# Performance work log

Measured on AMD Instinct MI355X. Metric: run time of the kernel, lower is better.

Reference implementation:

```python
import jax, jax.numpy as jnp
import numpy as np

EPS = 1e-5
LORA_DIM = 64
LORA_SCALE = LORA_DIM ** (-0.5)
GRAD_SCALE = 0.5  # infeat_grad_scale (bp_to_unet=True path)


def _ln(x, g=None, b=None):
    mu = jnp.mean(x, axis=-1, keepdims=True)
    var = jnp.mean((x - mu) ** 2, axis=-1, keepdims=True)
    y = (x - mu) * jax.lax.rsqrt(var + EPS)
    if g is not None:
        y = y * g + b
    return y


def _grad_scale(t, s=GRAD_SCALE):
    # identity in forward, scales gradient by s in backward
    return t * s + jax.lax.stop_gradient(t) * (1.0 - s)


def setup_inputs() -> dict:
    key = jax.random.key(0)
    ks = jax.random.split(key, 8)
    B, C, H, W = 32, 1280, 32, 32
    TD, LD = 768, LORA_DIM
    inp = {}
    inp["layer_infeat"] = jax.random.normal(ks[0], (B, C, H, W), jnp.float32)
    inp["layer_inquery"] = jax.random.normal(ks[1], (B, H * W, C), jnp.float32)
    inp["token_q_emb"] = jax.random.normal(ks[2], (TD,), jnp.float32)
    # learned params
    inp["to_q_w"] = jax.random.normal(ks[3], (C, TD), jnp.float32) * (TD ** -0.5)
    inp["ln_x_g"] = jnp.ones((C,), jnp.float32)
    inp["ln_x_b"] = jnp.zeros((C,), jnp.float32)
    inp["ln_k_g"] = jnp.ones((C,), jnp.float32)
    inp["ln_k_b"] = jnp.zeros((C,), jnp.float32)
    inp["ln_q_g"] = jnp.ones((TD,), jnp.float32)
    inp["ln_q_b"] = jnp.zeros((TD,), jnp.float32)
    inp["lora_q_w"] = jax.random.normal(ks[4], (LD, C), jnp.float32) * (C ** -0.5)
    inp["lora_k_w"] = jax.random.normal(ks[5], (LD, C), jnp.float32) * (C ** -0.5)
    inp["mask"] = jax.random.randint(ks[6], (B, 1, H, W), 0, 2).astype(jnp.float32)
    return inp


def reference(layer_infeat, layer_inquery, token_q_emb, to_q_w,
              ln_x_g, ln_x_b, ln_k_g, ln_k_b, ln_q_g, ln_q_b,
              lora_q_w, lora_k_w, mask):
    B, C, H, W = layer_infeat.shape
    # flatten(2).permute(0,2,1): [B,C,H,W] -> [B, HW, C]
    x = _grad_scale(layer_infeat).reshape(B, C, H * W).transpose(0, 2, 1)
    k_in = _grad_scale(layer_inquery)
    # q = to_q(ln_q(token_q_emb[None])) -> [1, C], broadcast to [B, 1, C]
    q = _ln(token_q_emb[None, :], ln_q_g, ln_q_b) @ to_q_w.T
    q = jnp.broadcast_to(q[None], (B, 1, C))
    k = _ln(k_in, ln_k_g, ln_k_b)   # [B, HW, C]
    v = _ln(x, ln_x_g, ln_x_b)      # [B, HW, C]
    # LoRA score path (use_lora=True since lora_dim>0)
    lora_q = _ln(q) @ lora_q_w.T    # [B, 1, LD]
    lora_k = _ln(k) @ lora_k_w.T    # [B, HW, LD]
    sim = jnp.einsum('bid,bjd->bij', lora_q, lora_k) * LORA_SCALE  # [B,1,HW]
    # mask: nearest interpolation to (H,W) is identity (same size); flatten
    m = mask.reshape(B, 1, H * W) > 0
    sim = jnp.where(m, sim, -jnp.finfo(sim.dtype).max)
    attn = jax.nn.softmax(sim, axis=-1)
    fg = jnp.einsum('bij,bjd->bid', attn, v)            # [B, 1, C]
    bg = jnp.mean(v, axis=1, keepdims=True) - fg        # [B, 1, C]
    out = jnp.concatenate([fg, bg], axis=-1)            # [B, 1, 2C]
    return out[:, 0, :]                                  # [B, 2C]
```

## Files before the change

### kernel.cpp

```cpp
#include <hip/hip_runtime.h>
#include <math.h>

#define B_   32
#define CD   1280
#define HW_  1024
#define TD_  768
#define LD_  64
#define EPSF 1e-5f
#define LORA_SCALE_F 0.125f

__device__ __forceinline__ float wredSum(float a) {
#pragma unroll
  for (int o = 32; o; o >>= 1) a += __shfl_xor(a, o, 64);
  return a;
}
__device__ __forceinline__ void wred2(float& a, float& b) {
#pragma unroll
  for (int o = 32; o; o >>= 1) { a += __shfl_xor(a, o, 64); b += __shfl_xor(b, o, 64); }
}
__device__ __forceinline__ float blockSum(float v, float* red) {
  int t = threadIdx.x;
  red[t] = v; __syncthreads();
#pragma unroll
  for (int s = 128; s > 0; s >>= 1) { if (t < s) red[t] += red[t + s]; __syncthreads(); }
  float r = red[0]; __syncthreads();
  return r;
}
__device__ __forceinline__ float blockMax(float v, float* red) {
  int t = threadIdx.x;
  red[t] = v; __syncthreads();
#pragma unroll
  for (int s = 128; s > 0; s >>= 1) { if (t < s) red[t] = fmaxf(red[t], red[t + s]); __syncthreads(); }
  float r = red[0]; __syncthreads();
  return r;
}
__device__ __forceinline__ void blockSum2(float& a, float& b, float2* red) {
  int t = threadIdx.x;
  red[t] = make_float2(a, b); __syncthreads();
#pragma unroll
  for (int s = 128; s > 0; s >>= 1) {
    if (t < s) { red[t].x += red[t + s].x; red[t].y += red[t + s].y; }
    __syncthreads();
  }
  a = red[0].x; b = red[0].y; __syncthreads();
}

__global__ __launch_bounds__(256) void kA12(const float* __restrict__ tq,
                                            const float* __restrict__ lng,
                                            const float* __restrict__ lnb,
                                            const float* __restrict__ to_q_w,
                                            float* __restrict__ q_out) {
  __shared__ float lnq[TD_];
  __shared__ float2 red[256];
  int t = threadIdx.x;
  float s = 0.f, ss = 0.f, vals[3];
#pragma unroll
  for (int k = 0; k < 3; k++) { float v = tq[t + 256 * k]; vals[k] = v; s += v; ss += v * v; }
  blockSum2(s, ss, red);
  float mu = s * (1.f / TD_);
  float r = rsqrtf(ss * (1.f / TD_) - mu * mu + EPSF);
#pragma unroll
  for (int k = 0; k < 3; k++) { int i = t + 256 * k; lnq[i] = (vals[k] - mu) * r * lng[i] + lnb[i]; }
  __syncthreads();
  int c = blockIdx.x * 4 + (t >> 6);
  int lane = t & 63;
  const float4* w4 = (const float4*)(to_q_w + (size_t)c * TD_);
  const float4* l4 = (const float4*)lnq;
  float dot = 0.f;
#pragma unroll
  for (int i = 0; i < 3; i++) {
    int f = i * 64 + lane;
    float4 w = w4[f], l = l4[f];
    dot += w.x * l.x + w.y * l.y + w.z * l.z + w.w * l.w;
  }
  dot = wredSum(dot);
  if (lane == 0) q_out[c] = dot;
}

__global__ __launch_bounds__(256) void kA34(const float* __restrict__ q_in,
                                            const float* __restrict__ lora_q_w,
                                            float* __restrict__ lq_out) {
  __shared__ float qs[CD];
  __shared__ float2 red[256];
  int t = threadIdx.x;
  float s = 0.f, ss = 0.f, vals[5];
#pragma unroll
  for (int k = 0; k < 5; k++) { float v = q_in[t + 256 * k]; vals[k] = v; s += v; ss += v * v; }
  blockSum2(s, ss, red);
  float mu = s * (1.f / CD);
  float r = rsqrtf(ss * (1.f / CD) - mu * mu + EPSF);
#pragma unroll
  for (int k = 0; k < 5; k++) { int i = t + 256 * k; qs[i] = (vals[k] - mu) * r; }
  __syncthreads();
  int d = blockIdx.x * 4 + (t >> 6);
  int lane = t & 63;
  const float4* w4 = (const float4*)(lora_q_w + (size_t)d * CD);
  const float4* q4 = (const float4*)qs;
  float dot = 0.f;
#pragma unroll
  for (int i = 0; i < 5; i++) {
    int f = i * 64 + lane;
    float4 w = w4[f], qq = q4[f];
    dot += w.x * qq.x + w.y * qq.y + w.z * qq.z + w.w * qq.w;
  }
  dot = wredSum(dot);
  if (lane == 0) lq_out[d] = dot;
}

__global__ __launch_bounds__(256) void kA56(const float* __restrict__ lq,
                                            const float* __restrict__ lora_k_w,
                                            float* __restrict__ w_eff) {
  __shared__ float l[LD_];
  int t = threadIdx.x;
  if (t < LD_) l[t] = lq[t];
  __syncthreads();
  int c = blockIdx.x * 256 + t;
  float acc = 0.f;
#pragma unroll 8
  for (int d = 0; d < LD_; d++) acc += l[d] * lora_k_w[(size_t)d * CD + c];
  w_eff[c] = acc;
}

__global__ __launch_bounds__(256) void kB(const float* __restrict__ kin,
                                          const float* __restrict__ g,
                                          const float* __restrict__ bb,
                                          const float* __restrict__ w_eff,
                                          float* __restrict__ sim) {
  __shared__ float4 gs[CD / 4], bs[CD / 4], ws[CD / 4];
  __shared__ float red[256];
  int t = threadIdx.x;
  float wsum = 0.f;
  for (int k = t; k < CD / 4; k += 256) {
    float4 w = ((const float4*)w_eff)[k];
    ws[k] = w;
    gs[k] = ((const float4*)g)[k];
    bs[k] = ((const float4*)bb)[k];
    wsum += w.x + w.y + w.z + w.w;
  }
  float W0 = blockSum(wsum, red);
  int wid = t >> 6, lane = t & 63;
  int gw = blockIdx.x * 4 + wid;
  for (int row = gw; row < B_ * HW_; row += 8192) {
    const float4* x4 = (const float4*)(kin + (size_t)row * CD);
    float4 xv[5];
    float s = 0.f, ss = 0.f;
#pragma unroll
    for (int i = 0; i < 5; i++) {
      float4 v = x4[i * 64 + lane];
      xv[i] = v;
      s += v.x + v.y + v.z + v.w;
      ss += v.x * v.x + v.y * v.y + v.z * v.z + v.w * v.w;
    }
    wred2(s, ss);
    float mu1 = s * (1.f / CD);
    float r1 = rsqrtf(ss * (1.f / CD) - mu1 * mu1 + EPSF);
    float s2 = 0.f, ss2 = 0.f;
#pragma unroll
    for (int i = 0; i < 5; i++) {
      int f = i * 64 + lane;
      float4 G = gs[f], Bv = bs[f], v = xv[i], kk;
      kk.x = (v.x - mu1) * r1 * G.x + Bv.x;
      kk.y = (v.y - mu1) * r1 * G.y + Bv.y;
      kk.z = (v.z - mu1) * r1 * G.z + Bv.z;
      kk.w = (v.w - mu1) * r1 * G.w + Bv.w;
      xv[i] = kk;
      s2 += kk.x + kk.y + kk.z + kk.w;
      ss2 += kk.x * kk.x + kk.y * kk.y + kk.z * kk.z + kk.w * kk.w;
    }
    wred2(s2, ss2);
    float mu2 = s2 * (1.f / CD);
    float r2 = rsqrtf(ss2 * (1.f / CD) - mu2 * mu2 + EPSF);
    float dot = 0.f;
#pragma unroll
    for (int i = 0; i < 5; i++) {
      float4 w = ws[i * 64 + lane], kk = xv[i];
      dot += w.x * kk.x + w.y * kk.y + w.z * kk.z + w.w * kk.w;
    }
    dot = wredSum(dot);
    if (lane == 0) sim[row] = LORA_SCALE_F * r2 * (dot - mu2 * W0);
  }
}

__global__ __launch_bounds__(256) void kD1(const float* __restrict__ infeat,
                                           float* __restrict__ mu_out,
                                           float* __restrict__ r_out) {
  int tile = blockIdx.x & 15, b = blockIdx.x >> 4;
  int t = threadIdx.x;
  int jg = t & 15;
  int slice = t >> 4;
  int j0 = tile * 64 + jg * 4;
  const float* base = infeat + (size_t)b * CD * HW_ + j0;
  float4 s = make_float4(0, 0, 0, 0), q = make_float4(0, 0, 0, 0);
  int c0 = slice * 80;
#pragma unroll 4
  for (int c = c0; c < c0 + 80; c++) {
    float4 v = *(const float4*)(base + (size_t)c * HW_);
    s.x += v.x; s.y += v.y; s.z += v.z; s.w += v.w;
    q.x += v.x * v.x; q.y += v.y * v.y; q.z += v.z * v.z; q.w += v.w * v.w;
  }
  __shared__ float4 sArr[16][16], qArr[16][16];
  sArr[slice][jg] = s; qArr[slice][jg] = q;
  __syncthreads();
#pragma unroll
  for (int st = 8; st > 0; st >>= 1) {
    if (slice < st) {
      float4 a = sArr[slice][jg], b2 = sArr[slice + st][jg];
      a.x += b2.x; a.y += b2.y; a.z += b2.z; a.w += b2.w;
      sArr[slice][jg] = a;
      a = qArr[slice][jg]; b2 = qArr[slice + st][jg];
      a.x += b2.x; a.y += b2.y; a.z += b2.z; a.w += b2.w;
      qArr[slice][jg] = a;
    }
    __syncthreads();
  }
  if (slice == 0) {
    float4 S = sArr[0][jg], Q = qArr[0][jg], mu, r;
    mu.x = S.x * (1.f / CD); mu.y = S.y * (1.f / CD);
    mu.z = S.z * (1.f / CD); mu.w = S.w * (1.f / CD);
    r.x = rsqrtf(Q.x * (1.f / CD) - mu.x * mu.x + EPSF);
    r.y = rsqrtf(Q.y * (1.f / CD) - mu.y * mu.y + EPSF);
    r.z = rsqrtf(Q.z * (1.f / CD) - mu.z * mu.z + EPSF);
    r.w = rsqrtf(Q.w * (1.f / CD) - mu.w * mu.w + EPSF);
    int j = b * HW_ + j0;
    *(float4*)(mu_out + j) = mu;
    *(float4*)(r_out + j) = r;
  }
}

__global__ __launch_bounds__(256) void kC(const float* __restrict__ sim,
                                          const float* __restrict__ mask,
                                          const float* __restrict__ mu,
                                          const float* __restrict__ r,
                                          float* __restrict__ w1,
                                          float* __restrict__ w2,
                                          float* __restrict__ S1,
                                          float* __restrict__ S3) {
  __shared__ float red[256];
  __shared__ float2 red2[256];
  int b = blockIdx.x, t = threadIdx.x;
  float4 sv = ((const float4*)(sim + b * HW_))[t];
  float4 mv = ((const float4*)(mask + b * HW_))[t];
  float4 muv = ((const float4*)(mu + b * HW_))[t];
  float4 rv = ((const float4*)(r + b * HW_))[t];
  const float NEG = -3.4028235e38f;
  float se0 = mv.x > 0.f ? sv.x : NEG;
  float se1 = mv.y > 0.f ? sv.y : NEG;
  float se2 = mv.z > 0.f ? sv.z : NEG;
  float se3 = mv.w > 0.f ? sv.w : NEG;
  float m = fmaxf(fmaxf(se0, se1), fmaxf(se2, se3));
  float M = blockMax(m, red);
  float e0 = expf(se0 - M), e1 = expf(se1 - M), e2 = expf(se2 - M), e3 = expf(se3 - M);
  float Z = blockSum(e0 + e1 + e2 + e3, red);
  float inv = 1.f / Z;
  float a0 = e0 * inv, a1 = e1 * inv, a2 = e2 * inv, a3 = e3 * inv;
  float4 w1v = make_float4(a0 * rv.x, a1 * rv.y, a2 * rv.z, a3 * rv.w);
  float4 w2v = make_float4(rv.x * (1.f / HW_), rv.y * (1.f / HW_),
                           rv.z * (1.f / HW_), rv.w * (1.f / HW_));
  float s1 = w1v.x * muv.x + w1v.y * muv.y + w1v.z * muv.z + w1v.w * muv.w;
  float s3 = w2v.x * muv.x + w2v.y * muv.y + w2v.z * muv.z + w2v.w * muv.w;
  blockSum2(s1, s3, red2);
  ((float4*)(w1 + b * HW_))[t] = w1v;
  ((float4*)(w2 + b * HW_))[t] = w2v;
  if (t == 0) { S1[b] = s1; S3[b] = s3; }
}

__global__ __launch_bounds__(256) void kD2(const float* __restrict__ infeat,
                                           const float* __restrict__ w1,
                                           const float* __restrict__ w2,
                                           const float* __restrict__ S1,
                                           const float* __restrict__ S3,
                                           const float* __restrict__ g,
                                           const float* __restrict__ bb,
                                           float* __restrict__ out) {
  __shared__ float4 w1s[HW_ / 4], w2s[HW_ / 4];
  int t = threadIdx.x;
  int b = blockIdx.x / 40, tile = blockIdx.x % 40;
  w1s[t] = ((const float4*)(w1 + b * HW_))[t];
  w2s[t] = ((const float4*)(w2 + b * HW_))[t];
  __syncthreads();
  int wid = t >> 6, lane = t & 63;
  float s1 = S1[b], s3 = S3[b];
#pragma unroll
  for (int k = 0; k < 8; k++) {
    int c = tile * 32 + wid * 8 + k;
    const float4* x4 = (const float4*)(infeat + (size_t)b * CD * HW_ + (size_t)c * HW_);
    float d1 = 0.f, d2 = 0.f;
#pragma unroll
    for (int i = 0; i < 4; i++) {
      int f = i * 64 + lane;
      float4 x = x4[f], a = w1s[f], w = w2s[f];
      d1 += x.x * a.x + x.y * a.y + x.z * a.z + x.w * a.w;
      d2 += x.x * w.x + x.y * w.y + x.z * w.z + x.w * w.w;
    }
    wred2(d1, d2);
    if (lane == 0) {
      float gc = g[c], bc = bb[c];
      float fg = gc * (d1 - s1) + bc;
      float vm = gc * (d2 - s3) + bc;
      out[(size_t)b * (2 * CD) + c] = fg;
      out[(size_t)b * (2 * CD) + CD + c] = vm - fg;
    }
  }
}

extern "C" void kernel_launch(void* const* d_in, const int* in_sizes, int n_in,
                              void* d_out, int out_size, void* d_ws, size_t ws_size,
                              hipStream_t stream) {
  const float* infeat  = (const float*)d_in[0];
  const float* inquery = (const float*)d_in[1];
  const float* tq      = (const float*)d_in[2];
  const float* to_q_w  = (const float*)d_in[3];
  const float* ln_x_g  = (const float*)d_in[4];
  const float* ln_x_b  = (const float*)d_in[5];
  const float* ln_k_g  = (const float*)d_in[6];
  const float* ln_k_b  = (const float*)d_in[7];
  const float* ln_q_g  = (const float*)d_in[8];
  const float* ln_q_b  = (const float*)d_in[9];
  const float* lora_q_w = (const float*)d_in[10];
  const float* lora_k_w = (const float*)d_in[11];
  const float* mask    = (const float*)d_in[12];
  float* out = (float*)d_out;

  float* ws = (float*)d_ws;
  float* q_ws    = ws;
  float* lq_ws   = ws + 1280;
  float* weff_ws = ws + 1344;
  float* sim_ws  = ws + 2624;
  float* mu_ws   = ws + 35392;
  float* r_ws    = ws + 68160;
  float* w1_ws   = ws + 100928;
  float* w2_ws   = ws + 133696;
  float* S1_ws   = ws + 166464;
  float* S3_ws   = ws + 166496;

  kA12<<<320, 256, 0, stream>>>(tq, ln_q_g, ln_q_b, to_q_w, q_ws);
  kA34<<<16, 256, 0, stream>>>(q_ws, lora_q_w, lq_ws);
  kA56<<<5, 256, 0, stream>>>(lq_ws, lora_k_w, weff_ws);
  kB<<<2048, 256, 0, stream>>>(inquery, ln_k_g, ln_k_b, weff_ws, sim_ws);
  kD1<<<512, 256, 0, stream>>>(infeat, mu_ws, r_ws);
  kC<<<32, 256, 0, stream>>>(sim_ws, mask, mu_ws, r_ws, w1_ws, w2_ws, S1_ws, S3_ws);
  kD2<<<1280, 256, 0, stream>>>(infeat, w1_ws, w2_ws, S1_ws, S3_ws, ln_x_g, ln_x_b, out);
}
```

Measured before the change: 405.7 us.

## Fuse small kernels: merge LoRA prep, co-schedule stats passes, fold softmax into final reduction

Merges the two LoRA projection kernels into one, in which each block recomputes the low-rank query vector. The key-path sim kernel and the infeat statistics kernel now run as one launch, split by block index, so the two independent memory-bound passes can overlap. The softmax/weight kernel is folded into the final reduction, with each of the 1280 blocks recomputing its batch's softmax weights in shared memory instead of reading them from a workspace. This cuts the launch count from seven to four and removes intermediate round trips, at the cost of redundant softmax and LoRA-q work per block.

```diff
diff --git a/kernel.cpp b/kernel.cpp
--- a/kernel.cpp
+++ b/kernel.cpp
@@ -18,19 +18,17 @@
 #pragma unroll
   for (int o = 32; o; o >>= 1) { a += __shfl_xor(a, o, 64); b += __shfl_xor(b, o, 64); }
 }
+__device__ __forceinline__ void wred3(float& a, float& b, float& c) {
+#pragma unroll
+  for (int o = 32; o; o >>= 1) {
+    a += __shfl_xor(a, o, 64); b += __shfl_xor(b, o, 64); c += __shfl_xor(c, o, 64);
+  }
+}
 __device__ __forceinline__ float blockSum(float v, float* red) {
   int t = threadIdx.x;
   red[t] = v; __syncthreads();
 #pragma unroll
   for (int s = 128; s > 0; s >>= 1) { if (t < s) red[t] += red[t + s]; __syncthreads(); }
-  float r = red[0]; __syncthreads();
-  return r;
-}
-__device__ __forceinline__ float blockMax(float v, float* red) {
-  int t = threadIdx.x;
-  red[t] = v; __syncthreads();
-#pragma unroll
-  for (int s = 128; s > 0; s >>= 1) { if (t < s) red[t] = fmaxf(red[t], red[t + s]); __syncthreads(); }
   float r = red[0]; __syncthreads();
   return r;
 }
@@ -77,167 +75,176 @@
   if (lane == 0) q_out[c] = dot;
 }
 
-__global__ __launch_bounds__(256) void kA34(const float* __restrict__ q_in,
-                                            const float* __restrict__ lora_q_w,
-                                            float* __restrict__ lq_out) {
-  __shared__ float qs[CD];
-  __shared__ float2 red[256];
-  int t = threadIdx.x;
+__global__ __launch_bounds__(256) void kA3456(const float* __restrict__ q_in,
+                                              const float* __restrict__ lora_q_w,
+                                              const float* __restrict__ lora_k_w,
+                                              float* __restrict__ w_eff) {
+  __shared__ float qn[CD];
+  __shared__ float lq[LD_];
+  __shared__ float redS[8];
+  int t = threadIdx.x;
+  int wid = t >> 6, lane = t & 63;
   float s = 0.f, ss = 0.f, vals[5];
 #pragma unroll
   for (int k = 0; k < 5; k++) { float v = q_in[t + 256 * k]; vals[k] = v; s += v; ss += v * v; }
-  blockSum2(s, ss, red);
+  wred2(s, ss);
+  if (lane == 0) { redS[wid * 2] = s; redS[wid * 2 + 1] = ss; }
+  __syncthreads();
+  s = redS[0] + redS[2] + redS[4] + redS[6];
+  ss = redS[1] + redS[3] + redS[5] + redS[7];
   float mu = s * (1.f / CD);
   float r = rsqrtf(ss * (1.f / CD) - mu * mu + EPSF);
 #pragma unroll
-  for (int k = 0; k < 5; k++) { int i = t + 256 * k; qs[i] = (vals[k] - mu) * r; }
-  __syncthreads();
-  int d = blockIdx.x * 4 + (t >> 6);
-  int lane = t & 63;
-  const float4* w4 = (const float4*)(lora_q_w + (size_t)d * CD);
-  const float4* q4 = (const float4*)qs;
-  float dot = 0.f;
-#pragma unroll
-  for (int i = 0; i < 5; i++) {
-    int f = i * 64 + lane;
-    float4 w = w4[f], qq = q4[f];
-    dot += w.x * qq.x + w.y * qq.y + w.z * qq.z + w.w * qq.w;
-  }
-  dot = wredSum(dot);
-  if (lane == 0) lq_out[d] = dot;
-}
-
-__global__ __launch_bounds__(256) void kA56(const float* __restrict__ lq,
-                                            const float* __restrict__ lora_k_w,
-                                            float* __restrict__ w_eff) {
-  __shared__ float l[LD_];
-  int t = threadIdx.x;
-  if (t < LD_) l[t] = lq[t];
+  for (int k = 0; k < 5; k++) { int i = t + 256 * k; qn[i] = (vals[k] - mu) * r; }
+  __syncthreads();
+  {
+    int g = t >> 2, sub = t & 3;
+    const float4* w4 = (const float4*)(lora_q_w + (size_t)g * CD);
+    const float4* q4 = (const float4*)qn;
+    float dot = 0.f;
+#pragma unroll 8
+    for (int i = 0; i < 80; i++) {
+      int f = i * 4 + sub;
+      float4 w = w4[f], qq = q4[f];
+      dot += w.x * qq.x + w.y * qq.y + w.z * qq.z + w.w * qq.w;
+    }
+    dot += __shfl_xor(dot, 1, 64);
+    dot += __shfl_xor(dot, 2, 64);
+    if (sub == 0) lq[g] = dot;
+  }
   __syncthreads();
   int c = blockIdx.x * 256 + t;
   float acc = 0.f;
 #pragma unroll 8
-  for (int d = 0; d < LD_; d++) acc += l[d] * lora_k_w[(size_t)d * CD + c];
+  for (int d = 0; d < LD_; d++) acc += lq[d] * lora_k_w[(size_t)d * CD + c];
   w_eff[c] = acc;
 }
 
-__global__ __launch_bounds__(256) void kB(const float* __restrict__ kin,
-                                          const float* __restrict__ g,
-                                          const float* __restrict__ bb,
-                                          const float* __restrict__ w_eff,
-                                          float* __restrict__ sim) {
-  __shared__ float4 gs[CD / 4], bs[CD / 4], ws[CD / 4];
-  __shared__ float red[256];
-  int t = threadIdx.x;
-  float wsum = 0.f;
-  for (int k = t; k < CD / 4; k += 256) {
-    float4 w = ((const float4*)w_eff)[k];
-    ws[k] = w;
-    gs[k] = ((const float4*)g)[k];
-    bs[k] = ((const float4*)bb)[k];
-    wsum += w.x + w.y + w.z + w.w;
-  }
-  float W0 = blockSum(wsum, red);
+__global__ __launch_bounds__(256) void kBD1(const float* __restrict__ kin,
+                                            const float* __restrict__ g,
+                                            const float* __restrict__ bb,
+                                            const float* __restrict__ w_eff,
+                                            float* __restrict__ sim,
+                                            const float* __restrict__ infeat,
+                                            float* __restrict__ mu_out,
+                                            float* __restrict__ r_out) {
+  __shared__ float4 smem[1024];
+  int t = threadIdx.x;
+  if (blockIdx.x < 2048) {
+    float4* gs = smem;
+    float4* bs = smem + 320;
+    float4* ws = smem + 640;
+    float* red = (float*)(smem + 960);
+    float wsum = 0.f;
+    for (int k = t; k < CD / 4; k += 256) {
+      float4 w = ((const float4*)w_eff)[k];
+      ws[k] = w;
+      gs[k] = ((const float4*)g)[k];
+      bs[k] = ((const float4*)bb)[k];
+      wsum += w.x + w.y + w.z + w.w;
+    }
+    float W0 = blockSum(wsum, red);
+    int wid = t >> 6, lane = t & 63;
+    int gw = blockIdx.x * 4 + wid;
+    for (int row = gw; row < B_ * HW_; row += 8192) {
+      const float4* x4 = (const float4*)(kin + (size_t)row * CD);
+      float4 xv[5];
+      float s = 0.f, ss = 0.f;
+#pragma unroll
+      for (int i = 0; i < 5; i++) {
+        float4 v = x4[i * 64 + lane];
+        xv[i] = v;
+        s += v.x + v.y + v.z + v.w;
+        ss += v.x * v.x + v.y * v.y + v.z * v.z + v.w * v.w;
+      }
+      wred2(s, ss);
+      float mu1 = s * (1.f / CD);
+      float r1 = rsqrtf(ss * (1.f / CD) - mu1 * mu1 + EPSF);
+      float s2 = 0.f, ss2 = 0.f;
+#pragma unroll
+      for (int i = 0; i < 5; i++) {
+        int f = i * 64 + lane;
+        float4 G = gs[f], Bv = bs[f], v = xv[i], kk;
+        kk.x = (v.x - mu1) * r1 * G.x + Bv.x;
+        kk.y = (v.y - mu1) * r1 * G.y + Bv.y;
+        kk.z = (v.z - mu1) * r1 * G.z + Bv.z;
+        kk.w = (v.w - mu1) * r1 * G.w + Bv.w;
+        xv[i] = kk;
+        s2 += kk.x + kk.y + kk.z + kk.w;
+        ss2 += kk.x * kk.x + kk.y * kk.y + kk.z * kk.z + kk.w * kk.w;
+      }
+      wred2(s2, ss2);
+      float mu2 = s2 * (1.f / CD);
+      float r2 = rsqrtf(ss2 * (1.f / CD) - mu2 * mu2 + EPSF);
+      float dot = 0.f;
+#pragma unroll
+      for (int i = 0; i < 5; i++) {
+        float4 w = ws[i * 64 + lane], kk = xv[i];
+        dot += w.x * kk.x + w.y * kk.y + w.z * kk.z + w.w * kk.w;
+      }
+      dot = wredSum(dot);
+      if (lane == 0) sim[row] = LORA_SCALE_F * r2 * (dot - mu2 * W0);
+    }
+  } else {
+    int blk = blockIdx.x - 2048;
+    int tile = blk & 15, b = blk >> 4;
+    int jg = t & 15;
+    int slice = t >> 4;
+    int j0 = tile * 64 + jg * 4;
+    const float* base = infeat + (size_t)b * CD * HW_ + j0;
+    float4 s = make_float4(0, 0, 0, 0), q = make_float4(0, 0, 0, 0);
+    int c0 = slice * 80;
+#pragma unroll 4
+    for (int c = c0; c < c0 + 80; c++) {
+      float4 v = *(const float4*)(base + (size_t)c * HW_);
+      s.x += v.x; s.y += v.y; s.z += v.z; s.w += v.w;
+      q.x += v.x * v.x; q.y += v.y * v.y; q.z += v.z * v.z; q.w += v.w * v.w;
+    }
+    float4* sArr = smem;
+    float4* qArr = smem + 256;
+    sArr[slice * 16 + jg] = s; qArr[slice * 16 + jg] = q;
+    __syncthreads();
+#pragma unroll
+    for (int st = 8; st > 0; st >>= 1) {
+      if (slice < st) {
+        float4 a = sArr[slice * 16 + jg], b2 = sArr[(slice + st) * 16 + jg];
+        a.x += b2.x; a.y += b2.y; a.z += b2.z; a.w += b2.w;
+        sArr[slice * 16 + jg] = a;
+        a = qArr[slice * 16 + jg]; b2 = qArr[(slice + st) * 16 + jg];
+        a.x += b2.x; a.y += b2.y; a.z += b2.z; a.w += b2.w;
+        qArr[slice * 16 + jg] = a;
+      }
+      __syncthreads();
+    }
+    if (slice == 0) {
+      float4 S = sArr[jg], Q = qArr[jg], mu, r;
+      mu.x = S.x * (1.f / CD); mu.y = S.y * (1.f / CD);
+      mu.z = S.z * (1.f / CD); mu.w = S.w * (1.f / CD);
+      r.x = rsqrtf(Q.x * (1.f / CD) - mu.x * mu.x + EPSF);
+      r.y = rsqrtf(Q.y * (1.f / CD) - mu.y * mu.y + EPSF);
+      r.z = rsqrtf(Q.z * (1.f / CD) - mu.z * mu.z + EPSF);
+      r.w = rsqrtf(Q.w * (1.f / CD) - mu.w * mu.w + EPSF);
+      int j = b * HW_ + j0;
+      *(float4*)(mu_out + j) = mu;
+      *(float4*)(r_out + j) = r;
+    }
+  }
+}
+
+__global__ __launch_bounds__(256) void kD2f(const float* __restrict__ infeat,
+                                            const float* __restrict__ sim,
+                                            const float* __restrict__ mask,
+                                            const float* __restrict__ mu,
+                                            const float* __restrict__ r,
+                                            const float* __restrict__ g,
+                                            const float* __restrict__ bb,
+                                            float* __restrict__ out) {
+  __shared__ float4 w1s[HW_ / 4], w2s[HW_ / 4];
+  __shared__ float red[16];
+  int t = threadIdx.x;
+  int b = blockIdx.x / 40, tile = blockIdx.x % 40;
   int wid = t >> 6, lane = t & 63;
-  int gw = blockIdx.x * 4 + wid;
-  for (int row = gw; row < B_ * HW_; row += 8192) {
-    const float4* x4 = (const float4*)(kin + (size_t)row * CD);
-    float4 xv[5];
-    float s = 0.f, ss = 0.f;
-#pragma unroll
-    for (int i = 0; i < 5; i++) {
-      float4 v = x4[i * 64 + lane];
-      xv[i] = v;
-      s += v.x + v.y + v.z + v.w;
-      ss += v.x * v.x + v.y * v.y + v.z * v.z + v.w * v.w;
-    }
-    wred2(s, ss);
-    float mu1 = s * (1.f / CD);
-    float r1 = rsqrtf(ss * (1.f / CD) - mu1 * mu1 + EPSF);
-    float s2 = 0.f, ss2 = 0.f;
-#pragma unroll
-    for (int i = 0; i < 5; i++) {
-      int f = i * 64 + lane;
-      float4 G = gs[f], Bv = bs[f], v = xv[i], kk;
-      kk.x = (v.x - mu1) * r1 * G.x + Bv.x;
-      kk.y = (v.y - mu1) * r1 * G.y + Bv.y;
-      kk.z = (v.z - mu1) * r1 * G.z + Bv.z;
-      kk.w = (v.w - mu1) * r1 * G.w + Bv.w;
-      xv[i] = kk;
-      s2 += kk.x + kk.y + kk.z + kk.w;
-      ss2 += kk.x * kk.x + kk.y * kk.y + kk.z * kk.z + kk.w * kk.w;
-    }
-    wred2(s2, ss2);
-    float mu2 = s2 * (1.f / CD);
-    float r2 = rsqrtf(ss2 * (1.f / CD) - mu2 * mu2 + EPSF);
-    float dot = 0.f;
-#pragma unroll
-    for (int i = 0; i < 5; i++) {
-      float4 w = ws[i * 64 + lane], kk = xv[i];
-      dot += w.x * kk.x + w.y * kk.y + w.z * kk.z + w.w * kk.w;
-    }
-    dot = wredSum(dot);
-    if (lane == 0) sim[row] = LORA_SCALE_F * r2 * (dot - mu2 * W0);
-  }
-}
-
-__global__ __launch_bounds__(256) void kD1(const float* __restrict__ infeat,
-                                           float* __restrict__ mu_out,
-                                           float* __restrict__ r_out) {
-  int tile = blockIdx.x & 15, b = blockIdx.x >> 4;
-  int t = threadIdx.x;
-  int jg = t & 15;
-  int slice = t >> 4;
-  int j0 = tile * 64 + jg * 4;
-  const float* base = infeat + (size_t)b * CD * HW_ + j0;
-  float4 s = make_float4(0, 0, 0, 0), q = make_float4(0, 0, 0, 0);
-  int c0 = slice * 80;
-#pragma unroll 4
-  for (int c = c0; c < c0 + 80; c++) {
-    float4 v = *(const float4*)(base + (size_t)c * HW_);
-    s.x += v.x; s.y += v.y; s.z += v.z; s.w += v.w;
-    q.x += v.x * v.x; q.y += v.y * v.y; q.z += v.z * v.z; q.w += v.w * v.w;
-  }
-  __shared__ float4 sArr[16][16], qArr[16][16];
-  sArr[slice][jg] = s; qArr[slice][jg] = q;
-  __syncthreads();
-#pragma unroll
-  for (int st = 8; st > 0; st >>= 1) {
-    if (slice < st) {
-      float4 a = sArr[slice][jg], b2 = sArr[slice + st][jg];
-      a.x += b2.x; a.y += b2.y; a.z += b2.z; a.w += b2.w;
-      sArr[slice][jg] = a;
-      a = qArr[slice][jg]; b2 = qArr[slice + st][jg];
-      a.x += b2.x; a.y += b2.y; a.z += b2.z; a.w += b2.w;
-      qArr[slice][jg] = a;
-    }
-    __syncthreads();
-  }
-  if (slice == 0) {
-    float4 S = sArr[0][jg], Q = qArr[0][jg], mu, r;
-    mu.x = S.x * (1.f / CD); mu.y = S.y * (1.f / CD);
-    mu.z = S.z * (1.f / CD); mu.w = S.w * (1.f / CD);
-    r.x = rsqrtf(Q.x * (1.f / CD) - mu.x * mu.x + EPSF);
-    r.y = rsqrtf(Q.y * (1.f / CD) - mu.y * mu.y + EPSF);
-    r.z = rsqrtf(Q.z * (1.f / CD) - mu.z * mu.z + EPSF);
-    r.w = rsqrtf(Q.w * (1.f / CD) - mu.w * mu.w + EPSF);
-    int j = b * HW_ + j0;
-    *(float4*)(mu_out + j) = mu;
-    *(float4*)(r_out + j) = r;
-  }
-}
-
-__global__ __launch_bounds__(256) void kC(const float* __restrict__ sim,
-                                          const float* __restrict__ mask,
-                                          const float* __restrict__ mu,
-                                          const float* __restrict__ r,
-                                          float* __restrict__ w1,
-                                          float* __restrict__ w2,
-                                          float* __restrict__ S1,
-                                          float* __restrict__ S3) {
-  __shared__ float red[256];
-  __shared__ float2 red2[256];
-  int b = blockIdx.x, t = threadIdx.x;
+
   float4 sv = ((const float4*)(sim + b * HW_))[t];
   float4 mv = ((const float4*)(mask + b * HW_))[t];
   float4 muv = ((const float4*)(mu + b * HW_))[t];
@@ -248,38 +255,30 @@
   float se2 = mv.z > 0.f ? sv.z : NEG;
   float se3 = mv.w > 0.f ? sv.w : NEG;
   float m = fmaxf(fmaxf(se0, se1), fmaxf(se2, se3));
-  float M = blockMax(m, red);
+#pragma unroll
+  for (int o = 32; o; o >>= 1) m = fmaxf(m, __shfl_xor(m, o, 64));
+  if (lane == 0) red[wid] = m;
+  __syncthreads();
+  float M = fmaxf(fmaxf(red[0], red[1]), fmaxf(red[2], red[3]));
   float e0 = expf(se0 - M), e1 = expf(se1 - M), e2 = expf(se2 - M), e3 = expf(se3 - M);
-  float Z = blockSum(e0 + e1 + e2 + e3, red);
+  float Z = e0 + e1 + e2 + e3;
+  float t1 = e0 * rv.x * muv.x + e1 * rv.y * muv.y + e2 * rv.z * muv.z + e3 * rv.w * muv.w;
+  float t3 = rv.x * muv.x + rv.y * muv.y + rv.z * muv.z + rv.w * muv.w;
+  wred3(Z, t1, t3);
+  __syncthreads();
+  if (lane == 0) { red[4 + wid * 3] = Z; red[5 + wid * 3] = t1; red[6 + wid * 3] = t3; }
+  __syncthreads();
+  Z  = red[4] + red[7] + red[10] + red[13];
+  t1 = red[5] + red[8] + red[11] + red[14];
+  t3 = red[6] + red[9] + red[12] + red[15];
   float inv = 1.f / Z;
-  float a0 = e0 * inv, a1 = e1 * inv, a2 = e2 * inv, a3 = e3 * inv;
-  float4 w1v = make_float4(a0 * rv.x, a1 * rv.y, a2 * rv.z, a3 * rv.w);
-  float4 w2v = make_float4(rv.x * (1.f / HW_), rv.y * (1.f / HW_),
-                           rv.z * (1.f / HW_), rv.w * (1.f / HW_));
-  float s1 = w1v.x * muv.x + w1v.y * muv.y + w1v.z * muv.z + w1v.w * muv.w;
-  float s3 = w2v.x * muv.x + w2v.y * muv.y + w2v.z * muv.z + w2v.w * muv.w;
-  blockSum2(s1, s3, red2);
-  ((float4*)(w1 + b * HW_))[t] = w1v;
-  ((float4*)(w2 + b * HW_))[t] = w2v;
-  if (t == 0) { S1[b] = s1; S3[b] = s3; }
-}
-
-__global__ __launch_bounds__(256) void kD2(const float* __restrict__ infeat,
-                                           const float* __restrict__ w1,
-                                           const float* __restrict__ w2,
-                                           const float* __restrict__ S1,
-                                           const float* __restrict__ S3,
-                                           const float* __restrict__ g,
-                                           const float* __restrict__ bb,
-                                           float* __restrict__ out) {
-  __shared__ float4 w1s[HW_ / 4], w2s[HW_ / 4];
-  int t = threadIdx.x;
-  int b = blockIdx.x / 40, tile = blockIdx.x % 40;
-  w1s[t] = ((const float4*)(w1 + b * HW_))[t];
-  w2s[t] = ((const float4*)(w2 + b * HW_))[t];
-  __syncthreads();
-  int wid = t >> 6, lane = t & 63;
-  float s1 = S1[b], s3 = S3[b];
+  float s1 = t1 * inv;
+  float s3 = t3 * (1.f / HW_);
+  w1s[t] = make_float4(e0 * rv.x * inv, e1 * rv.y * inv, e2 * rv.z * inv, e3 * rv.w * inv);
+  w2s[t] = make_float4(rv.x * (1.f / HW_), rv.y * (1.f / HW_),
+                       rv.z * (1.f / HW_), rv.w * (1.f / HW_));
+  __syncthreads();
+
 #pragma unroll
   for (int k = 0; k < 8; k++) {
     int c = tile * 32 + wid * 8 + k;
@@ -323,21 +322,15 @@
 
   float* ws = (float*)d_ws;
   float* q_ws    = ws;
-  float* lq_ws   = ws + 1280;
-  float* weff_ws = ws + 1344;
-  float* sim_ws  = ws + 2624;
-  float* mu_ws   = ws + 35392;
-  float* r_ws    = ws + 68160;
-  float* w1_ws   = ws + 100928;
-  float* w2_ws   = ws + 133696;
-  float* S1_ws   = ws + 166464;
-  float* S3_ws   = ws + 166496;
+  float* weff_ws = ws + 1280;
+  float* sim_ws  = ws + 2560;
+  float* mu_ws   = ws + 35328;
+  float* r_ws    = ws + 68096;
 
   kA12<<<320, 256, 0, stream>>>(tq, ln_q_g, ln_q_b, to_q_w, q_ws);
-  kA34<<<16, 256, 0, stream>>>(q_ws, lora_q_w, lq_ws);
-  kA56<<<5, 256, 0, stream>>>(lq_ws, lora_k_w, weff_ws);
-  kB<<<2048, 256, 0, stream>>>(inquery, ln_k_g, ln_k_b, weff_ws, sim_ws);
-  kD1<<<512, 256, 0, stream>>>(infeat, mu_ws, r_ws);
-  kC<<<32, 256, 0, stream>>>(sim_ws, mask, mu_ws, r_ws, w1_ws, w2_ws, S1_ws, S3_ws);
-  kD2<<<1280, 256, 0, stream>>>(infeat, w1_ws, w2_ws, S1_ws, S3_ws, ln_x_g, ln_x_b, out);
-}
+  kA3456<<<5, 256, 0, stream>>>(q_ws, lora_q_w, lora_k_w, weff_ws);
+  kBD1<<<2560, 256, 0, stream>>>(inquery, ln_k_g, ln_k_b, weff_ws, sim_ws,
+                                 infeat, mu_ws, r_ws);
+  kD2f<<<1280, 256, 0, stream>>>(infeat, sim_ws, mask, mu_ws, r_ws,
+                                 ln_x_g, ln_x_b, out);
+}
```

Result: no change. 406.5 us (+0.2%).
